# Kernel optimization log

Measured on AMD Instinct MI355X. Metric: run time of the kernel, lower is better.

## Reference

```python
import jax, jax.numpy as jnp
import numpy as np

B, T, N = 128, 32, 196
E = 1024   # embed dim
FD = 1024  # feature dim
H = 1024   # hidden size
A = 1024   # attention dim
SCALE = 0.02


def setup_inputs() -> dict:
    key = jax.random.key(0)
    ks = jax.random.split(key, 16)
    g = lambda k, shape: (jax.random.normal(k, shape, dtype=jnp.float32) * SCALE)
    return {
        "feats": jax.random.normal(ks[0], (B, N, FD), dtype=jnp.float32),
        "embeddings": jax.random.normal(ks[1], (B, T, E), dtype=jnp.float32),
        # additive attention params: v^T tanh(feats @ Wf + h @ Wh + b_att)
        "Wf": g(ks[2], (FD, A)),
        "Wh": g(ks[3], (H, A)),
        "b_att": jnp.zeros((A,), dtype=jnp.float32),
        "v": g(ks[4], (A,)),
        # layer-0 LSTMCell (input = concat(embed, attn) of size E+FD)
        "W_ih0": g(ks[5], (4 * H, E + FD)),
        "W_hh0": g(ks[6], (4 * H, H)),
        "b_ih0": jnp.zeros((4 * H,), dtype=jnp.float32),
        "b_hh0": jnp.zeros((4 * H,), dtype=jnp.float32),
        # layer-1 LSTMCell (input size H)
        "W_ih1": g(ks[7], (4 * H, H)),
        "W_hh1": g(ks[8], (4 * H, H)),
        "b_ih1": jnp.zeros((4 * H,), dtype=jnp.float32),
        "b_hh1": jnp.zeros((4 * H,), dtype=jnp.float32),
    }


def _lstm_cell(x, h, c, W_ih, W_hh, b_ih, b_hh):
    # PyTorch LSTMCell: gates ordered i, f, g, o
    gates = x @ W_ih.T + h @ W_hh.T + (b_ih + b_hh)
    i, f, g, o = jnp.split(gates, 4, axis=-1)
    c_new = jax.nn.sigmoid(f) * c + jax.nn.sigmoid(i) * jnp.tanh(g)
    h_new = jax.nn.sigmoid(o) * jnp.tanh(c_new)
    return h_new, c_new


def reference(feats, embeddings, Wf, Wh, b_att, v, W_ih0, W_hh0, b_ih0, b_hh0,
              W_ih1, W_hh1, b_ih1, b_hh1):
    Bb = embeddings.shape[0]
    # precompute the h-independent half of the attention energies: [B, N, A]
    f_proj = jnp.einsum("bnf,fa->bna", feats, Wf) + b_att

    h0 = jnp.zeros((Bb, H), dtype=feats.dtype)
    c0 = jnp.zeros((Bb, H), dtype=feats.dtype)

    def step(carry, embed_t):
        h0, c0 = carry
        # additive attention with query h0
        e = jnp.tanh(f_proj + (h0 @ Wh)[:, None, :])      # [B, N, A]
        scores = jnp.einsum("bna,a->bn", e, v)            # [B, N]
        alpha = jax.nn.softmax(scores, axis=-1)
        attn = jnp.einsum("bn,bnf->bf", alpha, feats)     # [B, FD]
        x = jnp.concatenate([embed_t, attn], axis=1)      # [B, E+FD]
        h0n, c0n = _lstm_cell(x, h0, c0, W_ih0, W_hh0, b_ih0, b_hh0)
        # faithful to source: layer 1 uses (h0n, c0n) as its state AND h0n as input
        h1, c1 = _lstm_cell(h0n, h0n, c0n, W_ih1, W_hh1, b_ih1, b_hh1)
        return (h0n, c0n), h1

    (_, _), outs = jax.lax.scan(step, (h0, c0), jnp.swapaxes(embeddings, 0, 1))
    return jnp.swapaxes(outs, 0, 1)  # [B, T, H]
```

## Files before the change

### kernel.cpp

```cpp
#include <hip/hip_runtime.h>
#include <hip/hip_cooperative_groups.h>
#include <cstddef>

typedef unsigned short ushort_t;
typedef unsigned int uint_t;
typedef __attribute__((ext_vector_type(8))) short bf16x8;
typedef __attribute__((ext_vector_type(4))) float f32x4;

constexpr int kB  = 128;
constexpr int kT  = 32;
constexpr int kN  = 196;
constexpr int kH  = 1024;

constexpr int ARENA_BYTES = 34816;

__device__ __forceinline__ float fsigmoid(float x) { return 1.f / (1.f + __expf(-x)); }
__device__ __forceinline__ float ftanh(float x)    { return 1.f - 2.f / (__expf(2.f * x) + 1.f); }
__device__ __forceinline__ ushort_t f2bf(float f) {
    uint_t u = __float_as_uint(f);
    return (ushort_t)((u + 0x7fffu + ((u >> 16) & 1u)) >> 16);
}

__global__ __launch_bounds__(256) void wf_transpose(
    const float* __restrict__ Wsrc, ushort_t* __restrict__ dst)
{
    __shared__ float t[64][65];
    const int k0 = blockIdx.x * 64, a0 = blockIdx.y * 64;
    const int c = threadIdx.x & 15, r0 = threadIdx.x >> 4;
#pragma unroll
    for (int i = 0; i < 4; ++i) {
        const int r = r0 + i * 16;
        const float4 v = *(const float4*)(Wsrc + (size_t)(k0 + r) * 1024 + a0 + c * 4);
        t[r][c * 4 + 0] = v.x; t[r][c * 4 + 1] = v.y;
        t[r][c * 4 + 2] = v.z; t[r][c * 4 + 3] = v.w;
    }
    __syncthreads();
#pragma unroll
    for (int i = 0; i < 4; ++i) {
        const int r = r0 + i * 16;
        ushort4 h;
        h.x = f2bf(t[c * 4 + 0][r]); h.y = f2bf(t[c * 4 + 1][r]);
        h.z = f2bf(t[c * 4 + 2][r]); h.w = f2bf(t[c * 4 + 3][r]);
        *(ushort4*)&dst[(size_t)(a0 + r) * 1024 + k0 + c * 4] = h;
    }
}

__global__ __launch_bounds__(256) void pack_whh0(
    const float* __restrict__ Whh0, ushort_t* __restrict__ Wbig)
{
    const int idx = blockIdx.x * 256 + threadIdx.x;
    const int j = idx >> 8, k4 = (idx & 255) * 4;
    const int u = j >> 2, g = j & 3;
    const float4 v = *(const float4*)(Whh0 + (size_t)(g * 1024 + u) * 1024 + k4);
    ushort4 h;
    h.x = f2bf(v.x); h.y = f2bf(v.y); h.z = f2bf(v.z); h.w = f2bf(v.w);
    *(ushort4*)&Wbig[(size_t)(1024 + j) * 1024 + k4] = h;
}

__global__ __launch_bounds__(256) void pack_w1sum(
    const float* __restrict__ Wih1, const float* __restrict__ Whh1,
    ushort_t* __restrict__ Wbig)
{
    const int idx = blockIdx.x * 256 + threadIdx.x;
    const int j = idx >> 8, k4 = (idx & 255) * 4;
    const int u = j >> 2, g = j & 3;
    const size_t o = (size_t)(g * 1024 + u) * 1024 + k4;
    const float4 a = *(const float4*)(Wih1 + o);
    const float4 b = *(const float4*)(Whh1 + o);
    ushort4 h;
    h.x = f2bf(a.x + b.x); h.y = f2bf(a.y + b.y);
    h.z = f2bf(a.z + b.z); h.w = f2bf(a.w + b.w);
    *(ushort4*)&Wbig[(size_t)(5120 + j) * 1024 + k4] = h;
}

__global__ __launch_bounds__(256) void pack_w0cat(
    const float* __restrict__ Wih0, ushort_t* __restrict__ W0cat)
{
    const int idx = blockIdx.x * 256 + threadIdx.x;
    const int j = idx >> 9, k4 = (idx & 511) * 4;
    const int u = j >> 2, g = j & 3;
    const int srccol = (k4 < 1024) ? (k4 + 1024) : (k4 - 1024);
    const float4 v = *(const float4*)(Wih0 + (size_t)(g * 1024 + u) * 2048 + srccol);
    ushort4 h;
    h.x = f2bf(v.x); h.y = f2bf(v.y); h.z = f2bf(v.z); h.w = f2bf(v.w);
    *(ushort4*)&W0cat[(size_t)j * 2048 + k4] = h;
}

__global__ __launch_bounds__(256) void cast_bf(
    const float* __restrict__ src, ushort_t* __restrict__ dst)
{
    const size_t idx = ((size_t)blockIdx.x * 256 + threadIdx.x) * 4;
    const float4 v = *(const float4*)(src + idx);
    ushort4 h;
    h.x = f2bf(v.x); h.y = f2bf(v.y); h.z = f2bf(v.z); h.w = f2bf(v.w);
    *(ushort4*)&dst[idx] = h;
}

template<int BF>
__global__ __launch_bounds__(256) void fproj_mfma(
    const float* __restrict__ featsf, const ushort_t* __restrict__ featsbf,
    const ushort_t* __restrict__ WfT,
    const float* __restrict__ bias, ushort_t* __restrict__ fprojbf)
{
    __shared__ alignas(16) char farena[40960];
    ushort_t* As = (ushort_t*)farena;
    ushort_t* Bs = As + 2 * 5120;
    ushort_t* Cs = (ushort_t*)farena;

    const int tid = threadIdx.x;
    const int n0 = blockIdx.x * 128, m0 = blockIdx.y * 128;
    const int lane = tid & 63, w = tid >> 6;
    const int wm = (w & 1) * 64, wn = (w >> 1) * 64;
    const int lr = lane & 15, quad = lane >> 4;

    const int xrow0 = tid >> 2, xrow1 = 64 + (tid >> 2);
    const int xkc = (tid & 3) * 8;

    f32x4 acc[4][4];
#pragma unroll
    for (int i = 0; i < 4; ++i)
#pragma unroll
        for (int j = 0; j < 4; ++j)
            acc[i][j] = (f32x4){0.f, 0.f, 0.f, 0.f};

    uint4 a0r, a1r, b0r, b1r;
    float4 f00, f01, f10, f11;

    auto LOAD = [&](int k0) {
        if (BF) {
            a0r = *(const uint4*)&featsbf[(size_t)(m0 + xrow0) * 1024 + k0 + xkc];
            a1r = *(const uint4*)&featsbf[(size_t)(m0 + xrow1) * 1024 + k0 + xkc];
        } else {
            f00 = *(const float4*)&featsf[(size_t)(m0 + xrow0) * 1024 + k0 + xkc];
            f01 = *(const float4*)&featsf[(size_t)(m0 + xrow0) * 1024 + k0 + xkc + 4];
            f10 = *(const float4*)&featsf[(size_t)(m0 + xrow1) * 1024 + k0 + xkc];
            f11 = *(const float4*)&featsf[(size_t)(m0 + xrow1) * 1024 + k0 + xkc + 4];
        }
        b0r = *(const uint4*)&WfT[(size_t)(n0 + xrow0) * 1024 + k0 + xkc];
        b1r = *(const uint4*)&WfT[(size_t)(n0 + xrow1) * 1024 + k0 + xkc];
    };
    auto WRITE = [&](int buf) {
        if (BF) {
            *(uint4*)&As[buf * 5120 + xrow0 * 40 + xkc] = a0r;
            *(uint4*)&As[buf * 5120 + xrow1 * 40 + xkc] = a1r;
        } else {
            ushort4 h;
            h.x = f2bf(f00.x); h.y = f2bf(f00.y); h.z = f2bf(f00.z); h.w = f2bf(f00.w);
            *(ushort4*)&As[buf * 5120 + xrow0 * 40 + xkc] = h;
            h.x = f2bf(f01.x); h.y = f2bf(f01.y); h.z = f2bf(f01.z); h.w = f2bf(f01.w);
            *(ushort4*)&As[buf * 5120 + xrow0 * 40 + xkc + 4] = h;
            h.x = f2bf(f10.x); h.y = f2bf(f10.y); h.z = f2bf(f10.z); h.w = f2bf(f10.w);
            *(ushort4*)&As[buf * 5120 + xrow1 * 40 + xkc] = h;
            h.x = f2bf(f11.x); h.y = f2bf(f11.y); h.z = f2bf(f11.z); h.w = f2bf(f11.w);
            *(ushort4*)&As[buf * 5120 + xrow1 * 40 + xkc + 4] = h;
        }
        *(uint4*)&Bs[buf * 5120 + xrow0 * 40 + xkc] = b0r;
        *(uint4*)&Bs[buf * 5120 + xrow1 * 40 + xkc] = b1r;
    };

    LOAD(0); WRITE(0); __syncthreads();
    int cur = 0;
    for (int k0 = 32; k0 <= 1024; k0 += 32) {
        const bool more = (k0 < 1024);
        if (more) LOAD(k0);
        bf16x8 af[4], bb[4];
#pragma unroll
        for (int mf = 0; mf < 4; ++mf)
            af[mf] = *(const bf16x8*)&As[cur * 5120 + (wm + mf * 16 + lr) * 40 + quad * 8];
#pragma unroll
        for (int nf = 0; nf < 4; ++nf)
            bb[nf] = *(const bf16x8*)&Bs[cur * 5120 + (wn + nf * 16 + lr) * 40 + quad * 8];
#pragma unroll
        for (int mf = 0; mf < 4; ++mf)
#pragma unroll
            for (int nf = 0; nf < 4; ++nf)
                acc[mf][nf] = __builtin_amdgcn_mfma_f32_16x16x32_bf16(
                    af[mf], bb[nf], acc[mf][nf], 0, 0, 0);
        if (more) WRITE(cur ^ 1);
        __syncthreads();
        cur ^= 1;
    }

#pragma unroll
    for (int nf = 0; nf < 4; ++nf) {
        const int n = wn + nf * 16 + lr;
        const float bn = bias[n0 + n];
#pragma unroll
        for (int mf = 0; mf < 4; ++mf)
#pragma unroll
            for (int r = 0; r < 4; ++r) {
                const int m = wm + mf * 16 + quad * 4 + r;
                Cs[m * 136 + n] = f2bf(acc[mf][nf][r] + bn);
            }
    }
    __syncthreads();
#pragma unroll
    for (int p = 0; p < 8; ++p) {
        const int row = p * 16 + (tid >> 4);
        const int c8 = (tid & 15) * 8;
        const uint4 v = *(const uint4*)&Cs[row * 136 + c8];
        *(uint4*)&fprojbf[(size_t)(m0 + row) * 1024 + n0 + c8] = v;
    }
}

__device__ __forceinline__ void phase_hgemm(
    char* arena, int job, int tstep,
    const ushort_t* __restrict__ hbf, const ushort_t* __restrict__ Wbig,
    const float* __restrict__ cbuf,
    const float* __restrict__ bih1, const float* __restrict__ bhh1,
    float* __restrict__ hwh, float* __restrict__ Ypart,
    float* __restrict__ out)
{
    ushort_t* xs  = (ushort_t*)arena;
    ushort_t* wsB = xs + 10240;
    float*    eps = (float*)arena;

    const int tid = threadIdx.x;
    const int n0 = job * 64;
    const int lane = tid & 63, w = tid >> 6;
    const int wm = (w & 1) * 64, wn = (w >> 1) * 32;
    const int lr = lane & 15, quad = lane >> 4;

    const int xrow0 = tid >> 2, xrow1 = 64 + (tid >> 2);
    const int xkc = (tid & 3) * 8;

    f32x4 acc[4][2];
#pragma unroll
    for (int i = 0; i < 4; ++i) {
        acc[i][0] = (f32x4){0.f, 0.f, 0.f, 0.f};
        acc[i][1] = (f32x4){0.f, 0.f, 0.f, 0.f};
    }

    uint4 x0r, x1r, w0r;
    auto LOAD = [&](int k0) {
        x0r = *(const uint4*)&hbf[(size_t)xrow0 * 1024 + k0 + xkc];
        x1r = *(const uint4*)&hbf[(size_t)xrow1 * 1024 + k0 + xkc];
        w0r = *(const uint4*)&Wbig[(size_t)(n0 + xrow0) * 1024 + k0 + xkc];
    };
    auto WRITE = [&](int buf) {
        *(uint4*)&xs[buf * 5120 + xrow0 * 40 + xkc] = x0r;
        *(uint4*)&xs[buf * 5120 + xrow1 * 40 + xkc] = x1r;
        *(uint4*)&wsB[buf * 2560 + xrow0 * 40 + xkc] = w0r;
    };

    LOAD(0); WRITE(0); __syncthreads();
    int cur = 0;
    for (int k0 = 32; k0 <= 1024; k0 += 32) {
        const bool more = (k0 < 1024);
        if (more) LOAD(k0);
        bf16x8 af[4], bb[2];
#pragma unroll
        for (int mf = 0; mf < 4; ++mf)
            af[mf] = *(const bf16x8*)&xs[cur * 5120 + (wm + mf * 16 + lr) * 40 + quad * 8];
#pragma unroll
        for (int nf = 0; nf < 2; ++nf)
            bb[nf] = *(const bf16x8*)&wsB[cur * 2560 + (wn + nf * 16 + lr) * 40 + quad * 8];
#pragma unroll
        for (int mf = 0; mf < 4; ++mf)
#pragma unroll
            for (int nf = 0; nf < 2; ++nf)
                acc[mf][nf] = __builtin_amdgcn_mfma_f32_16x16x32_bf16(
                    af[mf], bb[nf], acc[mf][nf], 0, 0, 0);
        if (more) WRITE(cur ^ 1);
        __syncthreads();
        cur ^= 1;
    }

    if (n0 < 5120) {
        float* dst = (n0 < 1024) ? hwh : Ypart;
        const int stride = (n0 < 1024) ? 1024 : 4096;
        const int nbase = (n0 < 1024) ? n0 : (n0 - 1024);
#pragma unroll
        for (int mf = 0; mf < 4; ++mf)
#pragma unroll
            for (int nf = 0; nf < 2; ++nf)
#pragma unroll
                for (int r = 0; r < 4; ++r) {
                    const int m = wm + mf * 16 + quad * 4 + r;
                    const int n = nbase + wn + nf * 16 + lr;
                    dst[(size_t)m * stride + n] = acc[mf][nf][r];
                }
    } else {
#pragma unroll
        for (int mf = 0; mf < 4; ++mf)
#pragma unroll
            for (int nf = 0; nf < 2; ++nf)
#pragma unroll
                for (int r = 0; r < 4; ++r)
                    eps[(wm + mf * 16 + quad * 4 + r) * 65 + (wn + nf * 16 + lr)] = acc[mf][nf][r];
        __syncthreads();
        if (tstep >= 1) {
#pragma unroll
            for (int i = 0; i < 8; ++i) {
                const int cid = i * 256 + tid;
                const int b = cid & 127, ulc = cid >> 7;
                const int u = ((n0 - 5120) >> 2) + ulc;
                const float iv = fsigmoid(eps[b * 65 + ulc * 4 + 0] + bih1[u]        + bhh1[u]);
                const float fv = fsigmoid(eps[b * 65 + ulc * 4 + 1] + bih1[1024 + u] + bhh1[1024 + u]);
                const float gv = ftanh   (eps[b * 65 + ulc * 4 + 2] + bih1[2048 + u] + bhh1[2048 + u]);
                const float ov = fsigmoid(eps[b * 65 + ulc * 4 + 3] + bih1[3072 + u] + bhh1[3072 + u]);
                const float cp = cbuf[(size_t)b * 1024 + u];
                const float cn = fv * cp + iv * gv;
                out[((size_t)b * kT + (tstep - 1)) * 1024 + u] = ov * ftanh(cn);
            }
        }
    }
}

__device__ __forceinline__ void phase_scores(
    int job,
    const ushort_t* __restrict__ fprojbf, const float* __restrict__ hwh,
    const float* __restrict__ vvec, float* __restrict__ scoresbuf)
{
    const int b = job & 127, chunk = job >> 7;
    const int tid = threadIdx.x, lane = tid & 63, w = tid >> 6;

    float hw[16], vr[16];
    {
        const int a0 = lane * 16;
#pragma unroll
        for (int q = 0; q < 4; ++q) {
            const float4 s0 = *(const float4*)(hwh + (size_t)b * 1024 + a0 + q * 4);
            hw[q * 4 + 0] = s0.x; hw[q * 4 + 1] = s0.y;
            hw[q * 4 + 2] = s0.z; hw[q * 4 + 3] = s0.w;
            const float4 vv = *(const float4*)(vvec + a0 + q * 4);
            vr[q * 4 + 0] = vv.x; vr[q * 4 + 1] = vv.y;
            vr[q * 4 + 2] = vv.z; vr[q * 4 + 3] = vv.w;
        }
    }

#pragma unroll
    for (int i = 0; i < 7; ++i) {
        const int n = chunk * 28 + w * 7 + i;
        const ushort_t* fp = fprojbf + ((size_t)(b * kN + n)) * 1024 + lane * 16;
        const uint4 u0 = *(const uint4*)(fp);
        const uint4 u1 = *(const uint4*)(fp + 8);
        float p = 0.f;
        const uint_t uu[8] = {u0.x, u0.y, u0.z, u0.w, u1.x, u1.y, u1.z, u1.w};
#pragma unroll
        for (int q = 0; q < 8; ++q) {
            const float xa = __uint_as_float(uu[q] << 16);
            const float xb = __uint_as_float(uu[q] & 0xffff0000u);
            p += ftanh(xa + hw[2 * q]) * vr[2 * q];
            p += ftanh(xb + hw[2 * q + 1]) * vr[2 * q + 1];
        }
#pragma unroll
        for (int off = 32; off; off >>= 1) p += __shfl_down(p, off);
        if (lane == 0) scoresbuf[b * kN + n] = p;
    }
}

__device__ __forceinline__ void phase_attn(
    char* arena, int job,
    const float* __restrict__ scoresbuf, const ushort_t* __restrict__ featsbf,
    ushort_t* __restrict__ attnbf)
{
    float* alpha_s = (float*)arena;
    float* red = alpha_s + 200;
    const int b = job >> 1;
    const int tid = threadIdx.x;

    const float val = (tid < kN) ? scoresbuf[b * kN + tid] : -1e30f;
    float m = val;
#pragma unroll
    for (int off = 32; off; off >>= 1) m = fmaxf(m, __shfl_down(m, off));
    if ((tid & 63) == 0) red[tid >> 6] = m;
    __syncthreads();
    m = fmaxf(fmaxf(red[0], red[1]), fmaxf(red[2], red[3]));
    const float e = (tid < kN) ? __expf(val - m) : 0.f;
    float s = e;
#pragma unroll
    for (int off = 32; off; off >>= 1) s += __shfl_down(s, off);
    if ((tid & 63) == 0) red[4 + (tid >> 6)] = s;
    __syncthreads();
    s = red[4] + red[5] + red[6] + red[7];
    if (tid < kN) alpha_s[tid] = e * (1.f / s);
    __syncthreads();

    const int f0 = (job & 1) * 512 + tid * 2;
    const ushort_t* fb = featsbf + (size_t)b * kN * 1024 + f0;
    float a0 = 0.f, a1 = 0.f;
#pragma unroll 4
    for (int n = 0; n < kN; ++n) {
        const uint_t u = *(const uint_t*)(fb + (size_t)n * 1024);
        a0 += alpha_s[n] * __uint_as_float(u << 16);
        a1 += alpha_s[n] * __uint_as_float(u & 0xffff0000u);
    }
    uint_t o = ((uint_t)f2bf(a1) << 16) | (uint_t)f2bf(a0);
    *(uint_t*)&attnbf[(size_t)b * 1024 + f0] = o;
}

__device__ __forceinline__ void phase_gates(
    char* arena, int job, int tstep,
    const ushort_t* __restrict__ attnbf, const ushort_t* __restrict__ embbf,
    const ushort_t* __restrict__ W0cat, const float* __restrict__ Ypart,
    const float* __restrict__ bih0, const float* __restrict__ bhh0,
    float* __restrict__ cbuf, ushort_t* __restrict__ hbf)
{
    ushort_t* xs  = (ushort_t*)arena;
    ushort_t* ws2 = xs + 10240;
    float*    eps = (float*)arena;

    const int tid = threadIdx.x;
    const int n0 = job * 32;
    const int lane = tid & 63, w = tid >> 6;
    const int wm = (w & 1) * 64, wn = (w >> 1) * 16;
    const int lr = lane & 15, quad = lane >> 4;

    const int xrow0 = tid >> 2, xrow1 = 64 + (tid >> 2);
    const int xkc = (tid & 3) * 8;
    const int wrow = tid >> 3, wkc = (tid & 7) * 4;

    f32x4 acc[4];
#pragma unroll
    for (int i = 0; i < 4; ++i) acc[i] = (f32x4){0.f, 0.f, 0.f, 0.f};

    uint4 x0r, x1r; uint2 w0r;
    auto LOAD = [&](int k0) {
        const ushort_t* s0 = (k0 < 1024)
            ? (attnbf + (size_t)xrow0 * 1024 + k0)
            : (embbf + ((size_t)xrow0 * kT + tstep) * 1024 + (k0 - 1024));
        const ushort_t* s1 = (k0 < 1024)
            ? (attnbf + (size_t)xrow1 * 1024 + k0)
            : (embbf + ((size_t)xrow1 * kT + tstep) * 1024 + (k0 - 1024));
        x0r = *(const uint4*)(s0 + xkc);
        x1r = *(const uint4*)(s1 + xkc);
        w0r = *(const uint2*)&W0cat[(size_t)(n0 + wrow) * 2048 + k0 + wkc];
    };
    auto WRITE = [&](int buf) {
        *(uint4*)&xs[buf * 5120 + xrow0 * 40 + xkc] = x0r;
        *(uint4*)&xs[buf * 5120 + xrow1 * 40 + xkc] = x1r;
        *(uint2*)&ws2[buf * 1280 + wrow * 40 + wkc] = w0r;
    };

    LOAD(0); WRITE(0); __syncthreads();
    int cur = 0;
    for (int k0 = 32; k0 <= 2048; k0 += 32) {
        const bool more = (k0 < 2048);
        if (more) LOAD(k0);
        bf16x8 af[4], bb;
#pragma unroll
        for (int mf = 0; mf < 4; ++mf)
            af[mf] = *(const bf16x8*)&xs[cur * 5120 + (wm + mf * 16 + lr) * 40 + quad * 8];
        bb = *(const bf16x8*)&ws2[cur * 1280 + (wn + lr) * 40 + quad * 8];
#pragma unroll
        for (int mf = 0; mf < 4; ++mf)
            acc[mf] = __builtin_amdgcn_mfma_f32_16x16x32_bf16(
                af[mf], bb, acc[mf], 0, 0, 0);
        if (more) WRITE(cur ^ 1);
        __syncthreads();
        cur ^= 1;
    }

#pragma unroll
    for (int mf = 0; mf < 4; ++mf)
#pragma unroll
        for (int r = 0; r < 4; ++r)
            eps[(wm + mf * 16 + quad * 4 + r) * 33 + wn + lr] = acc[mf][r];
    __syncthreads();

#pragma unroll
    for (int i = 0; i < 4; ++i) {
        const int cid = i * 256 + tid;
        const int b = cid & 127, ulc = cid >> 7;
        const int u = (n0 >> 2) + ulc;
        const int jb = n0 + ulc * 4;
        const float* yp = Ypart + (size_t)b * 4096 + jb;
        const float iv = fsigmoid(eps[b * 33 + ulc * 4 + 0] + yp[0] + bih0[u]        + bhh0[u]);
        const float fv = fsigmoid(eps[b * 33 + ulc * 4 + 1] + yp[1] + bih0[1024 + u] + bhh0[1024 + u]);
        const float gv = ftanh   (eps[b * 33 + ulc * 4 + 2] + yp[2] + bih0[2048 + u] + bhh0[2048 + u]);
        const float ov = fsigmoid(eps[b * 33 + ulc * 4 + 3] + yp[3] + bih0[3072 + u] + bhh0[3072 + u]);
        const float cp = cbuf[(size_t)b * 1024 + u];
        const float cn = fv * cp + iv * gv;
        cbuf[(size_t)b * 1024 + u] = cn;
        hbf[(size_t)b * 1024 + u] = f2bf(ov * ftanh(cn));
    }
}

__global__ __launch_bounds__(256) void hgemm_A(
    const ushort_t* __restrict__ hbf, const ushort_t* __restrict__ Wbig,
    const float* __restrict__ cbuf,
    const float* __restrict__ bih1, const float* __restrict__ bhh1,
    float* __restrict__ hwh, float* __restrict__ Ypart,
    float* __restrict__ out, int tstep)
{
    __shared__ alignas(16) char arena[ARENA_BYTES];
    phase_hgemm(arena, blockIdx.x, tstep, hbf, Wbig, cbuf, bih1, bhh1, hwh, Ypart, out);
}

__global__ __launch_bounds__(256) void scores_kernel(
    const ushort_t* __restrict__ fprojbf, const float* __restrict__ hwh,
    const float* __restrict__ vvec, float* __restrict__ scoresbuf)
{
    phase_scores(blockIdx.x + 128 * blockIdx.y, fprojbf, hwh, vvec, scoresbuf);
}

template<int BF>
__global__ __launch_bounds__(256) void attn_kernel(
    const float* __restrict__ scoresbuf, const float* __restrict__ featsf,
    const ushort_t* __restrict__ featsbf, ushort_t* __restrict__ attnbf)
{
    __shared__ float alpha_s[200];
    __shared__ float red[8];
    const int b = blockIdx.x;
    const int tid = threadIdx.x;

    const float val = (tid < kN) ? scoresbuf[b * kN + tid] : -1e30f;
    float m = val;
#pragma unroll
    for (int off = 32; off; off >>= 1) m = fmaxf(m, __shfl_down(m, off));
    if ((tid & 63) == 0) red[tid >> 6] = m;
    __syncthreads();
    m = fmaxf(fmaxf(red[0], red[1]), fmaxf(red[2], red[3]));
    const float e = (tid < kN) ? __expf(val - m) : 0.f;
    float s = e;
#pragma unroll
    for (int off = 32; off; off >>= 1) s += __shfl_down(s, off);
    if ((tid & 63) == 0) red[4 + (tid >> 6)] = s;
    __syncthreads();
    s = red[4] + red[5] + red[6] + red[7];
    if (tid < kN) alpha_s[tid] = e * (1.f / s);
    __syncthreads();

    if (BF) {
        const int f0 = blockIdx.y * 512 + tid * 2;
        const ushort_t* fb = featsbf + (size_t)b * kN * 1024 + f0;
        float a0 = 0.f, a1 = 0.f;
#pragma unroll 4
        for (int n = 0; n < kN; ++n) {
            const uint_t u = *(const uint_t*)(fb + (size_t)n * 1024);
            a0 += alpha_s[n] * __uint_as_float(u << 16);
            a1 += alpha_s[n] * __uint_as_float(u & 0xffff0000u);
        }
        uint_t o = ((uint_t)f2bf(a1) << 16) | (uint_t)f2bf(a0);
        *(uint_t*)&attnbf[(size_t)b * 1024 + f0] = o;
    } else {
        const int f = blockIdx.y * 256 + tid;
        const float* fb = featsf + (size_t)b * kN * 1024 + f;
        float a = 0.f;
#pragma unroll 4
        for (int n = 0; n < kN; ++n) a += alpha_s[n] * fb[(size_t)n * 1024];
        attnbf[(size_t)b * 1024 + f] = f2bf(a);
    }
}

__global__ __launch_bounds__(256) void gatesC(
    const ushort_t* __restrict__ attnbf, const ushort_t* __restrict__ embbf,
    const ushort_t* __restrict__ W0cat, const float* __restrict__ Ypart,
    const float* __restrict__ bih0, const float* __restrict__ bhh0,
    float* __restrict__ cbuf, ushort_t* __restrict__ hbf, int tstep)
{
    __shared__ alignas(16) char arena[ARENA_BYTES];
    phase_gates(arena, blockIdx.x, tstep, attnbf, embbf, W0cat, Ypart,
                bih0, bhh0, cbuf, hbf);
}

__global__ __launch_bounds__(256, 2) void mega_kernel(
    ushort_t* hbf, const ushort_t* Wbig, float* cbuf,
    const float* bih1, const float* bhh1,
    float* hwh, float* Ypart, float* out,
    const ushort_t* fprojbf, const float* vvec, float* scoresbuf,
    const ushort_t* featsbf, ushort_t* attnbf,
    const ushort_t* embbf, const ushort_t* W0cat,
    const float* bih0, const float* bhh0)
{
    __shared__ alignas(16) char arena[ARENA_BYTES];
    cooperative_groups::grid_group grid = cooperative_groups::this_grid();
    const int blk = blockIdx.x;

    for (int t = 0; t < kT; ++t) {
        if (blk < 144)
            phase_hgemm(arena, blk, t, hbf, Wbig, cbuf, bih1, bhh1, hwh, Ypart, out);
        grid.sync();
        for (int j = blk; j < 896; j += 512)
            phase_scores(j, fprojbf, hwh, vvec, scoresbuf);
        grid.sync();
        if (blk < 256)
            phase_attn(arena, blk, scoresbuf, featsbf, attnbf);
        grid.sync();
        if (blk < 128)
            phase_gates(arena, blk, t, attnbf, embbf, W0cat, Ypart,
                        bih0, bhh0, cbuf, hbf);
        grid.sync();
    }
    if (blk < 64)
        phase_hgemm(arena, 80 + blk, kT, hbf, Wbig, cbuf, bih1, bhh1, hwh, Ypart, out);
}

extern "C" void kernel_launch(void* const* d_in, const int* in_sizes, int n_in,
                              void* d_out, int out_size, void* d_ws, size_t ws_size,
                              hipStream_t stream)
{
    const float* feats = (const float*)d_in[0];
    const float* emb   = (const float*)d_in[1];
    const float* Wf    = (const float*)d_in[2];
    const float* Wh    = (const float*)d_in[3];
    const float* b_att = (const float*)d_in[4];
    const float* vvec  = (const float*)d_in[5];
    const float* Wih0  = (const float*)d_in[6];
    const float* Whh0  = (const float*)d_in[7];
    const float* bih0  = (const float*)d_in[8];
    const float* bhh0  = (const float*)d_in[9];
    const float* Wih1  = (const float*)d_in[10];
    const float* Whh1  = (const float*)d_in[11];
    const float* bih1  = (const float*)d_in[12];
    const float* bhh1  = (const float*)d_in[13];
    float* out = (float*)d_out;

    ushort_t* fprojbf = (ushort_t*)d_ws;
    ushort_t* embbf   = fprojbf + (size_t)25088 * 1024;
    ushort_t* Wbig    = embbf   + (size_t)4096 * 1024;
    ushort_t* W0cat   = Wbig    + (size_t)9216 * 1024;
    ushort_t* WfT     = W0cat   + (size_t)4096 * 2048;
    ushort_t* hbf     = WfT     + (size_t)1024 * 1024;
    ushort_t* attnbf  = hbf     + (size_t)128 * 1024;
    float* hwh        = (float*)(attnbf + (size_t)128 * 1024);
    float* Ypart      = hwh   + (size_t)128 * 1024;
    float* cbuf       = Ypart + (size_t)128 * 4096;
    float* scoresbuf  = cbuf  + (size_t)128 * 1024;
    ushort_t* featsbf = (ushort_t*)(scoresbuf + 128 * 196);

    const size_t need_full = 152668160;
    const bool use_bf = (ws_size >= need_full);

    hipMemsetAsync(hbf, 0, sizeof(ushort_t) * 128 * 1024, stream);
    hipMemsetAsync(cbuf, 0, sizeof(float) * 128 * 1024, stream);

    wf_transpose<<<dim3(16, 16), 256, 0, stream>>>(Wf, WfT);
    wf_transpose<<<dim3(16, 16), 256, 0, stream>>>(Wh, Wbig);
    pack_whh0<<<4096, 256, 0, stream>>>(Whh0, Wbig);
    pack_w1sum<<<4096, 256, 0, stream>>>(Wih1, Whh1, Wbig);
    pack_w0cat<<<8192, 256, 0, stream>>>(Wih0, W0cat);
    cast_bf<<<4096, 256, 0, stream>>>(emb, embbf);
    if (use_bf) cast_bf<<<25088, 256, 0, stream>>>(feats, featsbf);

    if (use_bf)
        fproj_mfma<1><<<dim3(8, 196), 256, 0, stream>>>(feats, featsbf, WfT, b_att, fprojbf);
    else
        fproj_mfma<0><<<dim3(8, 196), 256, 0, stream>>>(feats, featsbf, WfT, b_att, fprojbf);

    bool did_coop = false;
    if (use_bf) {
        static int coop_ok = -1;
        if (coop_ok < 0) {
            int dev = 0; (void)hipGetDevice(&dev);
            int coop = 0;
            (void)hipDeviceGetAttribute(&coop, hipDeviceAttributeCooperativeLaunch, dev);
            int ncu = 0;
            (void)hipDeviceGetAttribute(&ncu, hipDeviceAttributeMultiprocessorCount, dev);
            int maxb = 0;
            hipError_t oe = hipOccupancyMaxActiveBlocksPerMultiprocessor(
                &maxb, mega_kernel, 256, 0);
            coop_ok = (coop != 0 && oe == hipSuccess && (long)maxb * ncu >= 512) ? 1 : 0;
        }
        if (coop_ok) {
            void* kargs[] = {
                (void*)&hbf, (void*)&Wbig, (void*)&cbuf, (void*)&bih1, (void*)&bhh1,
                (void*)&hwh, (void*)&Ypart, (void*)&out, (void*)&fprojbf, (void*)&vvec,
                (void*)&scoresbuf, (void*)&featsbf, (void*)&attnbf, (void*)&embbf,
                (void*)&W0cat, (void*)&bih0, (void*)&bhh0 };
            hipError_t le = hipLaunchCooperativeKernel(
                mega_kernel, dim3(512), dim3(256), kargs, 0u, stream);
            did_coop = (le == hipSuccess);
        }
    }

    if (!did_coop) {
        for (int t = 0; t < kT; ++t) {
            hgemm_A<<<144, 256, 0, stream>>>(hbf, Wbig, cbuf, bih1, bhh1,
                                             hwh, Ypart, out, t);
            scores_kernel<<<dim3(128, 7), 256, 0, stream>>>(fprojbf, hwh, vvec, scoresbuf);
            if (use_bf)
                attn_kernel<1><<<dim3(128, 2), 256, 0, stream>>>(scoresbuf, feats, featsbf, attnbf);
            else
                attn_kernel<0><<<dim3(128, 4), 256, 0, stream>>>(scoresbuf, feats, featsbf, attnbf);
            gatesC<<<128, 256, 0, stream>>>(attnbf, embbf, W0cat, Ypart,
                                            bih0, bhh0, cbuf, hbf, t);
        }
        hgemm_A<<<144, 256, 0, stream>>>(hbf, Wbig, cbuf, bih1, bhh1,
                                         hwh, Ypart, out, kT);
    }

    (void)in_sizes; (void)n_in; (void)out_size; (void)ws_size;
}
```

Measured before the change: 3.225 ms.

## Replace cooperative mega-kernel with per-step launches, fused scores+attn, K=64 tiles

```diff
diff --git a/kernel.cpp b/kernel.cpp
--- a/kernel.cpp
+++ b/kernel.cpp
@@ -1,5 +1,4 @@
 #include <hip/hip_runtime.h>
-#include <hip/hip_cooperative_groups.h>
 #include <cstddef>
 
 typedef unsigned short ushort_t;
@@ -12,7 +11,7 @@
 constexpr int kN  = 196;
 constexpr int kH  = 1024;
 
-constexpr int ARENA_BYTES = 34816;
+constexpr int ARENA_BYTES = 55296;
 
 __device__ __forceinline__ float fsigmoid(float x) { return 1.f / (1.f + __expf(-x)); }
 __device__ __forceinline__ float ftanh(float x)    { return 1.f - 2.f / (__expf(2.f * x) + 1.f); }
@@ -212,7 +211,7 @@
     float* __restrict__ out)
 {
     ushort_t* xs  = (ushort_t*)arena;
-    ushort_t* wsB = xs + 10240;
+    ushort_t* wsB = xs + 2 * 9216;
     float*    eps = (float*)arena;
 
     const int tid = threadIdx.x;
@@ -221,8 +220,8 @@
     const int wm = (w & 1) * 64, wn = (w >> 1) * 32;
     const int lr = lane & 15, quad = lane >> 4;
 
-    const int xrow0 = tid >> 2, xrow1 = 64 + (tid >> 2);
-    const int xkc = (tid & 3) * 8;
+    const int arow = tid >> 1, acol = (tid & 1) * 32;
+    const int wrow = tid >> 2, wcol = (tid & 3) * 16;
 
     f32x4 acc[4][2];
 #pragma unroll
@@ -231,36 +230,47 @@
         acc[i][1] = (f32x4){0.f, 0.f, 0.f, 0.f};
     }
 
-    uint4 x0r, x1r, w0r;
+    uint4 xr[4], wr[2];
     auto LOAD = [&](int k0) {
-        x0r = *(const uint4*)&hbf[(size_t)xrow0 * 1024 + k0 + xkc];
-        x1r = *(const uint4*)&hbf[(size_t)xrow1 * 1024 + k0 + xkc];
-        w0r = *(const uint4*)&Wbig[(size_t)(n0 + xrow0) * 1024 + k0 + xkc];
+#pragma unroll
+        for (int j = 0; j < 4; ++j)
+            xr[j] = *(const uint4*)&hbf[(size_t)arow * 1024 + k0 + acol + j * 8];
+#pragma unroll
+        for (int j = 0; j < 2; ++j)
+            wr[j] = *(const uint4*)&Wbig[(size_t)(n0 + wrow) * 1024 + k0 + wcol + j * 8];
     };
     auto WRITE = [&](int buf) {
-        *(uint4*)&xs[buf * 5120 + xrow0 * 40 + xkc] = x0r;
-        *(uint4*)&xs[buf * 5120 + xrow1 * 40 + xkc] = x1r;
-        *(uint4*)&wsB[buf * 2560 + xrow0 * 40 + xkc] = w0r;
+#pragma unroll
+        for (int j = 0; j < 4; ++j)
+            *(uint4*)&xs[buf * 9216 + arow * 72 + acol + j * 8] = xr[j];
+#pragma unroll
+        for (int j = 0; j < 2; ++j)
+            *(uint4*)&wsB[buf * 4608 + wrow * 72 + wcol + j * 8] = wr[j];
     };
 
     LOAD(0); WRITE(0); __syncthreads();
     int cur = 0;
-    for (int k0 = 32; k0 <= 1024; k0 += 32) {
+    for (int k0 = 64; k0 <= 1024; k0 += 64) {
         const bool more = (k0 < 1024);
         if (more) LOAD(k0);
-        bf16x8 af[4], bb[2];
-#pragma unroll
-        for (int mf = 0; mf < 4; ++mf)
-            af[mf] = *(const bf16x8*)&xs[cur * 5120 + (wm + mf * 16 + lr) * 40 + quad * 8];
-#pragma unroll
-        for (int nf = 0; nf < 2; ++nf)
-            bb[nf] = *(const bf16x8*)&wsB[cur * 2560 + (wn + nf * 16 + lr) * 40 + quad * 8];
-#pragma unroll
-        for (int mf = 0; mf < 4; ++mf)
+        bf16x8 af[2][4], bb[2][2];
+#pragma unroll
+        for (int ks = 0; ks < 2; ++ks) {
+#pragma unroll
+            for (int mf = 0; mf < 4; ++mf)
+                af[ks][mf] = *(const bf16x8*)&xs[cur * 9216 + (wm + mf * 16 + lr) * 72 + ks * 32 + quad * 8];
 #pragma unroll
             for (int nf = 0; nf < 2; ++nf)
-                acc[mf][nf] = __builtin_amdgcn_mfma_f32_16x16x32_bf16(
-                    af[mf], bb[nf], acc[mf][nf], 0, 0, 0);
+                bb[ks][nf] = *(const bf16x8*)&wsB[cur * 4608 + (wn + nf * 16 + lr) * 72 + ks * 32 + quad * 8];
+        }
+#pragma unroll
+        for (int ks = 0; ks < 2; ++ks)
+#pragma unroll
+            for (int mf = 0; mf < 4; ++mf)
+#pragma unroll
+                for (int nf = 0; nf < 2; ++nf)
+                    acc[mf][nf] = __builtin_amdgcn_mfma_f32_16x16x32_bf16(
+                        af[ks][mf], bb[ks][nf], acc[mf][nf], 0, 0, 0);
         if (more) WRITE(cur ^ 1);
         __syncthreads();
         cur ^= 1;
@@ -307,16 +317,31 @@
     }
 }
 
-__device__ __forceinline__ void phase_scores(
-    int job,
+__global__ __launch_bounds__(256) void hgemm_A(
+    const ushort_t* __restrict__ hbf, const ushort_t* __restrict__ Wbig,
+    const float* __restrict__ cbuf,
+    const float* __restrict__ bih1, const float* __restrict__ bhh1,
+    float* __restrict__ hwh, float* __restrict__ Ypart,
+    float* __restrict__ out, int tstep, int job_base)
+{
+    __shared__ alignas(16) char arena[ARENA_BYTES];
+    phase_hgemm(arena, blockIdx.x + job_base, tstep, hbf, Wbig, cbuf,
+                bih1, bhh1, hwh, Ypart, out);
+}
+
+__global__ __launch_bounds__(1024) void scores_attn(
     const ushort_t* __restrict__ fprojbf, const float* __restrict__ hwh,
-    const float* __restrict__ vvec, float* __restrict__ scoresbuf)
-{
-    const int b = job & 127, chunk = job >> 7;
+    const float* __restrict__ vvec, const ushort_t* __restrict__ featsbf,
+    ushort_t* __restrict__ attnbf)
+{
+    __shared__ float scores_s[196];
+    __shared__ float alpha_s[200];
+    __shared__ float red[32];
+    const int b = blockIdx.x;
     const int tid = threadIdx.x, lane = tid & 63, w = tid >> 6;
 
-    float hw[16], vr[16];
     {
+        float hw[16], vr[16];
         const int a0 = lane * 16;
 #pragma unroll
         for (int q = 0; q < 4; ++q) {
@@ -327,6 +352,81 @@
             vr[q * 4 + 0] = vv.x; vr[q * 4 + 1] = vv.y;
             vr[q * 4 + 2] = vv.z; vr[q * 4 + 3] = vv.w;
         }
+        for (int n = w; n < kN; n += 16) {
+            const ushort_t* fp = fprojbf + ((size_t)(b * kN + n)) * 1024 + lane * 16;
+            const uint4 u0 = *(const uint4*)(fp);
+            const uint4 u1 = *(const uint4*)(fp + 8);
+            float p = 0.f;
+            const uint_t uu[8] = {u0.x, u0.y, u0.z, u0.w, u1.x, u1.y, u1.z, u1.w};
+#pragma unroll
+            for (int q = 0; q < 8; ++q) {
+                const float xa = __uint_as_float(uu[q] << 16);
+                const float xb = __uint_as_float(uu[q] & 0xffff0000u);
+                p += ftanh(xa + hw[2 * q]) * vr[2 * q];
+                p += ftanh(xb + hw[2 * q + 1]) * vr[2 * q + 1];
+            }
+#pragma unroll
+            for (int off = 32; off; off >>= 1) p += __shfl_down(p, off);
+            if (lane == 0) scores_s[n] = p;
+        }
+    }
+    __syncthreads();
+
+    const float val = (tid < kN) ? scores_s[tid] : -1e30f;
+    float m = val;
+#pragma unroll
+    for (int off = 32; off; off >>= 1) m = fmaxf(m, __shfl_down(m, off));
+    if (lane == 0) red[w] = m;
+    __syncthreads();
+    m = red[0];
+#pragma unroll
+    for (int i = 1; i < 16; ++i) m = fmaxf(m, red[i]);
+    const float e = (tid < kN) ? __expf(val - m) : 0.f;
+    float s = e;
+#pragma unroll
+    for (int off = 32; off; off >>= 1) s += __shfl_down(s, off);
+    if (lane == 0) red[16 + w] = s;
+    __syncthreads();
+    s = red[16];
+#pragma unroll
+    for (int i = 1; i < 16; ++i) s += red[16 + i];
+    if (tid < kN) alpha_s[tid] = e * (1.f / s);
+    __syncthreads();
+
+    if (tid < 512) {
+        const int f0 = tid * 2;
+        const ushort_t* fb = featsbf + (size_t)b * kN * 1024 + f0;
+        float a0 = 0.f, a1 = 0.f;
+#pragma unroll 4
+        for (int n = 0; n < kN; ++n) {
+            const uint_t u = *(const uint_t*)(fb + (size_t)n * 1024);
+            a0 += alpha_s[n] * __uint_as_float(u << 16);
+            a1 += alpha_s[n] * __uint_as_float(u & 0xffff0000u);
+        }
+        uint_t o = ((uint_t)f2bf(a1) << 16) | (uint_t)f2bf(a0);
+        *(uint_t*)&attnbf[(size_t)b * 1024 + f0] = o;
+    }
+}
+
+__global__ __launch_bounds__(256) void scores_kernel(
+    const ushort_t* __restrict__ fprojbf, const float* __restrict__ hwh,
+    const float* __restrict__ vvec, float* __restrict__ scoresbuf)
+{
+    const int b = blockIdx.x, chunk = blockIdx.y;
+    const int tid = threadIdx.x, lane = tid & 63, w = tid >> 6;
+
+    float hw[16], vr[16];
+    {
+        const int a0 = lane * 16;
+#pragma unroll
+        for (int q = 0; q < 4; ++q) {
+            const float4 s0 = *(const float4*)(hwh + (size_t)b * 1024 + a0 + q * 4);
+            hw[q * 4 + 0] = s0.x; hw[q * 4 + 1] = s0.y;
+            hw[q * 4 + 2] = s0.z; hw[q * 4 + 3] = s0.w;
+            const float4 vv = *(const float4*)(vvec + a0 + q * 4);
+            vr[q * 4 + 0] = vv.x; vr[q * 4 + 1] = vv.y;
+            vr[q * 4 + 2] = vv.z; vr[q * 4 + 3] = vv.w;
+        }
     }
 
 #pragma unroll
@@ -350,14 +450,13 @@
     }
 }
 
-__device__ __forceinline__ void phase_attn(
-    char* arena, int job,
-    const float* __restrict__ scoresbuf, const ushort_t* __restrict__ featsbf,
+__global__ __launch_bounds__(256) void attn_kernel_f32(
+    const float* __restrict__ scoresbuf, const float* __restrict__ featsf,
     ushort_t* __restrict__ attnbf)
 {
-    float* alpha_s = (float*)arena;
-    float* red = alpha_s + 200;
-    const int b = job >> 1;
+    __shared__ float alpha_s[200];
+    __shared__ float red[8];
+    const int b = blockIdx.x;
     const int tid = threadIdx.x;
 
     const float val = (tid < kN) ? scoresbuf[b * kN + tid] : -1e30f;
@@ -377,17 +476,12 @@
     if (tid < kN) alpha_s[tid] = e * (1.f / s);
     __syncthreads();
 
-    const int f0 = (job & 1) * 512 + tid * 2;
-    const ushort_t* fb = featsbf + (size_t)b * kN * 1024 + f0;
-    float a0 = 0.f, a1 = 0.f;
+    const int f = blockIdx.y * 256 + tid;
+    const float* fb = featsf + (size_t)b * kN * 1024 + f;
+    float a = 0.f;
 #pragma unroll 4
-    for (int n = 0; n < kN; ++n) {
-        const uint_t u = *(const uint_t*)(fb + (size_t)n * 1024);
-        a0 += alpha_s[n] * __uint_as_float(u << 16);
-        a1 += alpha_s[n] * __uint_as_float(u & 0xffff0000u);
-    }
-    uint_t o = ((uint_t)f2bf(a1) << 16) | (uint_t)f2bf(a0);
-    *(uint_t*)&attnbf[(size_t)b * 1024 + f0] = o;
+    for (int n = 0; n < kN; ++n) a += alpha_s[n] * fb[(size_t)n * 1024];
+    attnbf[(size_t)b * 1024 + f] = f2bf(a);
 }
 
 __device__ __forceinline__ void phase_gates(
@@ -398,7 +492,7 @@
     float* __restrict__ cbuf, ushort_t* __restrict__ hbf)
 {
     ushort_t* xs  = (ushort_t*)arena;
-    ushort_t* ws2 = xs + 10240;
+    ushort_t* ws2 = xs + 2 * 9216;
     float*    eps = (float*)arena;
 
     const int tid = threadIdx.x;
@@ -407,46 +501,49 @@
     const int wm = (w & 1) * 64, wn = (w >> 1) * 16;
     const int lr = lane & 15, quad = lane >> 4;
 
-    const int xrow0 = tid >> 2, xrow1 = 64 + (tid >> 2);
-    const int xkc = (tid & 3) * 8;
-    const int wrow = tid >> 3, wkc = (tid & 7) * 4;
+    const int arow = tid >> 1, acol = (tid & 1) * 32;
+    const int wrow = tid >> 3, wcol = (tid & 7) * 8;
 
     f32x4 acc[4];
 #pragma unroll
     for (int i = 0; i < 4; ++i) acc[i] = (f32x4){0.f, 0.f, 0.f, 0.f};
 
-    uint4 x0r, x1r; uint2 w0r;
+    uint4 xr[4], wr;
     auto LOAD = [&](int k0) {
-        const ushort_t* s0 = (k0 < 1024)
-            ? (attnbf + (size_t)xrow0 * 1024 + k0)
-            : (embbf + ((size_t)xrow0 * kT + tstep) * 1024 + (k0 - 1024));
-        const ushort_t* s1 = (k0 < 1024)
-            ? (attnbf + (size_t)xrow1 * 1024 + k0)
-            : (embbf + ((size_t)xrow1 * kT + tstep) * 1024 + (k0 - 1024));
-        x0r = *(const uint4*)(s0 + xkc);
-        x1r = *(const uint4*)(s1 + xkc);
-        w0r = *(const uint2*)&W0cat[(size_t)(n0 + wrow) * 2048 + k0 + wkc];
+        const ushort_t* srcbase = (k0 < 1024)
+            ? (attnbf + (size_t)arow * 1024 + k0)
+            : (embbf + ((size_t)arow * kT + tstep) * 1024 + (k0 - 1024));
+#pragma unroll
+        for (int j = 0; j < 4; ++j)
+            xr[j] = *(const uint4*)(srcbase + acol + j * 8);
+        wr = *(const uint4*)&W0cat[(size_t)(n0 + wrow) * 2048 + k0 + wcol];
     };
     auto WRITE = [&](int buf) {
-        *(uint4*)&xs[buf * 5120 + xrow0 * 40 + xkc] = x0r;
-        *(uint4*)&xs[buf * 5120 + xrow1 * 40 + xkc] = x1r;
-        *(uint2*)&ws2[buf * 1280 + wrow * 40 + wkc] = w0r;
+#pragma unroll
+        for (int j = 0; j < 4; ++j)
+            *(uint4*)&xs[buf * 9216 + arow * 72 + acol + j * 8] = xr[j];
+        *(uint4*)&ws2[buf * 2304 + wrow * 72 + wcol] = wr;
     };
 
     LOAD(0); WRITE(0); __syncthreads();
     int cur = 0;
-    for (int k0 = 32; k0 <= 2048; k0 += 32) {
+    for (int k0 = 64; k0 <= 2048; k0 += 64) {
         const bool more = (k0 < 2048);
         if (more) LOAD(k0);
-        bf16x8 af[4], bb;
-#pragma unroll
-        for (int mf = 0; mf < 4; ++mf)
-            af[mf] = *(const bf16x8*)&xs[cur * 5120 + (wm + mf * 16 + lr) * 40 + quad * 8];
-        bb = *(const bf16x8*)&ws2[cur * 1280 + (wn + lr) * 40 + quad * 8];
-#pragma unroll
-        for (int mf = 0; mf < 4; ++mf)
-            acc[mf] = __builtin_amdgcn_mfma_f32_16x16x32_bf16(
-                af[mf], bb, acc[mf], 0, 0, 0);
+        bf16x8 af[2][4], bb[2];
+#pragma unroll
+        for (int ks = 0; ks < 2; ++ks) {
+#pragma unroll
+            for (int mf = 0; mf < 4; ++mf)
+                af[ks][mf] = *(const bf16x8*)&xs[cur * 9216 + (wm + mf * 16 + lr) * 72 + ks * 32 + quad * 8];
+            bb[ks] = *(const bf16x8*)&ws2[cur * 2304 + (wn + lr) * 72 + ks * 32 + quad * 8];
+        }
+#pragma unroll
+        for (int ks = 0; ks < 2; ++ks)
+#pragma unroll
+            for (int mf = 0; mf < 4; ++mf)
+                acc[mf] = __builtin_amdgcn_mfma_f32_16x16x32_bf16(
+                    af[ks][mf], bb[ks], acc[mf], 0, 0, 0);
         if (more) WRITE(cur ^ 1);
         __syncthreads();
         cur ^= 1;
@@ -477,73 +574,6 @@
     }
 }
 
-__global__ __launch_bounds__(256) void hgemm_A(
-    const ushort_t* __restrict__ hbf, const ushort_t* __restrict__ Wbig,
-    const float* __restrict__ cbuf,
-    const float* __restrict__ bih1, const float* __restrict__ bhh1,
-    float* __restrict__ hwh, float* __restrict__ Ypart,
-    float* __restrict__ out, int tstep)
-{
-    __shared__ alignas(16) char arena[ARENA_BYTES];
-    phase_hgemm(arena, blockIdx.x, tstep, hbf, Wbig, cbuf, bih1, bhh1, hwh, Ypart, out);
-}
-
-__global__ __launch_bounds__(256) void scores_kernel(
-    const ushort_t* __restrict__ fprojbf, const float* __restrict__ hwh,
-    const float* __restrict__ vvec, float* __restrict__ scoresbuf)
-{
-    phase_scores(blockIdx.x + 128 * blockIdx.y, fprojbf, hwh, vvec, scoresbuf);
-}
-
-template<int BF>
-__global__ __launch_bounds__(256) void attn_kernel(
-    const float* __restrict__ scoresbuf, const float* __restrict__ featsf,
-    const ushort_t* __restrict__ featsbf, ushort_t* __restrict__ attnbf)
-{
-    __shared__ float alpha_s[200];
-    __shared__ float red[8];
-    const int b = blockIdx.x;
-    const int tid = threadIdx.x;
-
-    const float val = (tid < kN) ? scoresbuf[b * kN + tid] : -1e30f;
-    float m = val;
-#pragma unroll
-    for (int off = 32; off; off >>= 1) m = fmaxf(m, __shfl_down(m, off));
-    if ((tid & 63) == 0) red[tid >> 6] = m;
-    __syncthreads();
-    m = fmaxf(fmaxf(red[0], red[1]), fmaxf(red[2], red[3]));
-    const float e = (tid < kN) ? __expf(val - m) : 0.f;
-    float s = e;
-#pragma unroll
-    for (int off = 32; off; off >>= 1) s += __shfl_down(s, off);
-    if ((tid & 63) == 0) red[4 + (tid >> 6)] = s;
-    __syncthreads();
-    s = red[4] + red[5] + red[6] + red[7];
-    if (tid < kN) alpha_s[tid] = e * (1.f / s);
-    __syncthreads();
-
-    if (BF) {
-        const int f0 = blockIdx.y * 512 + tid * 2;
-        const ushort_t* fb = featsbf + (size_t)b * kN * 1024 + f0;
-        float a0 = 0.f, a1 = 0.f;
-#pragma unroll 4
-        for (int n = 0; n < kN; ++n) {
-            const uint_t u = *(const uint_t*)(fb + (size_t)n * 1024);
-            a0 += alpha_s[n] * __uint_as_float(u << 16);
-            a1 += alpha_s[n] * __uint_as_float(u & 0xffff0000u);
-        }
-        uint_t o = ((uint_t)f2bf(a1) << 16) | (uint_t)f2bf(a0);
-        *(uint_t*)&attnbf[(size_t)b * 1024 + f0] = o;
-    } else {
-        const int f = blockIdx.y * 256 + tid;
-        const float* fb = featsf + (size_t)b * kN * 1024 + f;
-        float a = 0.f;
-#pragma unroll 4
-        for (int n = 0; n < kN; ++n) a += alpha_s[n] * fb[(size_t)n * 1024];
-        attnbf[(size_t)b * 1024 + f] = f2bf(a);
-    }
-}
-
 __global__ __launch_bounds__(256) void gatesC(
     const ushort_t* __restrict__ attnbf, const ushort_t* __restrict__ embbf,
     const ushort_t* __restrict__ W0cat, const float* __restrict__ Ypart,
@@ -553,38 +583,6 @@
     __shared__ alignas(16) char arena[ARENA_BYTES];
     phase_gates(arena, blockIdx.x, tstep, attnbf, embbf, W0cat, Ypart,
                 bih0, bhh0, cbuf, hbf);
-}
-
-__global__ __launch_bounds__(256, 2) void mega_kernel(
-    ushort_t* hbf, const ushort_t* Wbig, float* cbuf,
-    const float* bih1, const float* bhh1,
-    float* hwh, float* Ypart, float* out,
-    const ushort_t* fprojbf, const float* vvec, float* scoresbuf,
-    const ushort_t* featsbf, ushort_t* attnbf,
-    const ushort_t* embbf, const ushort_t* W0cat,
-    const float* bih0, const float* bhh0)
-{
-    __shared__ alignas(16) char arena[ARENA_BYTES];
-    cooperative_groups::grid_group grid = cooperative_groups::this_grid();
-    const int blk = blockIdx.x;
-
-    for (int t = 0; t < kT; ++t) {
-        if (blk < 144)
-            phase_hgemm(arena, blk, t, hbf, Wbig, cbuf, bih1, bhh1, hwh, Ypart, out);
-        grid.sync();
-        for (int j = blk; j < 896; j += 512)
-            phase_scores(j, fprojbf, hwh, vvec, scoresbuf);
-        grid.sync();
-        if (blk < 256)
-            phase_attn(arena, blk, scoresbuf, featsbf, attnbf);
-        grid.sync();
-        if (blk < 128)
-            phase_gates(arena, blk, t, attnbf, embbf, W0cat, Ypart,
-                        bih0, bhh0, cbuf, hbf);
-        grid.sync();
-    }
-    if (blk < 64)
-        phase_hgemm(arena, 80 + blk, kT, hbf, Wbig, cbuf, bih1, bhh1, hwh, Ypart, out);
 }
 
 extern "C" void kernel_launch(void* const* d_in, const int* in_sizes, int n_in,
@@ -639,47 +637,20 @@
     else
         fproj_mfma<0><<<dim3(8, 196), 256, 0, stream>>>(feats, featsbf, WfT, b_att, fprojbf);
 
-    bool did_coop = false;
-    if (use_bf) {
-        static int coop_ok = -1;
-        if (coop_ok < 0) {
-            int dev = 0; (void)hipGetDevice(&dev);
-            int coop = 0;
-            (void)hipDeviceGetAttribute(&coop, hipDeviceAttributeCooperativeLaunch, dev);
-            int ncu = 0;
-            (void)hipDeviceGetAttribute(&ncu, hipDeviceAttributeMultiprocessorCount, dev);
-            int maxb = 0;
-            hipError_t oe = hipOccupancyMaxActiveBlocksPerMultiprocessor(
-                &maxb, mega_kernel, 256, 0);
-            coop_ok = (coop != 0 && oe == hipSuccess && (long)maxb * ncu >= 512) ? 1 : 0;
-        }
-        if (coop_ok) {
-            void* kargs[] = {
-                (void*)&hbf, (void*)&Wbig, (void*)&cbuf, (void*)&bih1, (void*)&bhh1,
-                (void*)&hwh, (void*)&Ypart, (void*)&out, (void*)&fprojbf, (void*)&vvec,
-                (void*)&scoresbuf, (void*)&featsbf, (void*)&attnbf, (void*)&embbf,
-                (void*)&W0cat, (void*)&bih0, (void*)&bhh0 };
-            hipError_t le = hipLaunchCooperativeKernel(
-                mega_kernel, dim3(512), dim3(256), kargs, 0u, stream);
-            did_coop = (le == hipSuccess);
-        }
-    }
-
-    if (!did_coop) {
-        for (int t = 0; t < kT; ++t) {
-            hgemm_A<<<144, 256, 0, stream>>>(hbf, Wbig, cbuf, bih1, bhh1,
-                                             hwh, Ypart, out, t);
+    for (int t = 0; t < kT; ++t) {
+        hgemm_A<<<144, 256, 0, stream>>>(hbf, Wbig, cbuf, bih1, bhh1,
+                                         hwh, Ypart, out, t, 0);
+        if (use_bf) {
+            scores_attn<<<128, 1024, 0, stream>>>(fprojbf, hwh, vvec, featsbf, attnbf);
+        } else {
             scores_kernel<<<dim3(128, 7), 256, 0, stream>>>(fprojbf, hwh, vvec, scoresbuf);
-            if (use_bf)
-                attn_kernel<1><<<dim3(128, 2), 256, 0, stream>>>(scoresbuf, feats, featsbf, attnbf);
-            else
-                attn_kernel<0><<<dim3(128, 4), 256, 0, stream>>>(scoresbuf, feats, featsbf, attnbf);
-            gatesC<<<128, 256, 0, stream>>>(attnbf, embbf, W0cat, Ypart,
-                                            bih0, bhh0, cbuf, hbf, t);
-        }
-        hgemm_A<<<144, 256, 0, stream>>>(hbf, Wbig, cbuf, bih1, bhh1,
-                                         hwh, Ypart, out, kT);
-    }
+            attn_kernel_f32<<<dim3(128, 4), 256, 0, stream>>>(scoresbuf, feats, attnbf);
+        }
+        gatesC<<<128, 256, 0, stream>>>(attnbf, embbf, W0cat, Ypart,
+                                        bih0, bhh0, cbuf, hbf, t);
+    }
+    hgemm_A<<<64, 256, 0, stream>>>(hbf, Wbig, cbuf, bih1, bhh1,
+                                    hwh, Ypart, out, kT, 80);
 
     (void)in_sizes; (void)n_in; (void)out_size; (void)ws_size;
 }
```

Measured after the change: 4.048 ms. +25.5%, slower.
